# Kernel tuning notes

Measured on AMD Instinct MI355X. Metric: run time of the kernel, lower is better.

The kernel has to match this reference:

```python
import jax, jax.numpy as jnp
import numpy as np

B, S, E, H = 2, 2048, 1024, 16
D = E // H
LN_EPS = 1e-5
NORM_EPS = 1e-12  # F.normalize clamp_min


def setup_inputs() -> dict:
    key = jax.random.key(0)
    ks = jax.random.split(key, 4)
    x = jax.random.normal(ks[0], (B, S, E), dtype=jnp.float32)
    qkv_w = jax.random.normal(ks[1], (3 * E, E), dtype=jnp.float32) * 0.02
    qkv_b = jnp.zeros((3 * E,), dtype=jnp.float32)
    out_w = jax.random.normal(ks[2], (E, E), dtype=jnp.float32) * 0.02
    out_b = jnp.zeros((E,), dtype=jnp.float32)
    ln_w = jnp.ones((E,), dtype=jnp.float32)
    ln_b = jnp.zeros((E,), dtype=jnp.float32)
    qknorm_scale = jnp.asarray(E ** -0.5, dtype=jnp.float32)
    # RotaryEmbedding buffer: inv_freq interleaved (emb[::2] = emb[1::2] = base**(-arange(0,E,2)/E))
    base_freq = 10000.0 ** (-(np.arange(0, E, 2).astype(np.float32) / E))
    emb = np.empty((E,), dtype=np.float32)
    emb[::2] = base_freq
    emb[1::2] = base_freq
    inv_freq = jnp.asarray(emb)
    return {"x": x, "ln_w": ln_w, "ln_b": ln_b, "qkv_w": qkv_w, "qkv_b": qkv_b,
            "qknorm_scale": qknorm_scale, "out_w": out_w, "out_b": out_b, "inv_freq": inv_freq}


def _rotate(t, sin, cos):
    # Faithful to source: x1 = even idx (excluding last), x2 = odd idx; cat(-x2, x1)
    x1 = t[..., :-1:2]
    x2 = t[..., 1::2]
    t_rot = jnp.concatenate((-x2, x1), axis=-1)
    return t * cos + t_rot * sin


def _l2norm(t):
    n = jnp.sqrt(jnp.sum(t * t, axis=-1, keepdims=True))
    return t / jnp.maximum(n, NORM_EPS)


def reference(x, ln_w, ln_b, qkv_w, qkv_b, qknorm_scale, out_w, out_b, inv_freq):
    # --- prenorm (LayerNorm, eps=1e-5) ---
    mu = jnp.mean(x, axis=-1, keepdims=True)
    var = jnp.mean((x - mu) ** 2, axis=-1, keepdims=True)
    xn = (x - mu) / jnp.sqrt(var + LN_EPS) * ln_w + ln_b
    # --- QKV projection ---
    qkv = xn @ qkv_w.T + qkv_b  # [B,S,3E]
    q, k, v = jnp.split(qkv, 3, axis=-1)
    # --- rotary (source uses scalar seq*inv_freq, not per-position) ---
    seq = q.shape[1]
    sin = jnp.sin(seq * inv_freq)
    cos = jnp.cos(seq * inv_freq)
    q = _rotate(q, sin, cos)
    k = _rotate(k, sin, cos)
    # --- split heads: [B,S,E] -> [B,H,S,D] ---
    split = lambda t: t.reshape(B, seq, H, D).transpose(0, 2, 1, 3)
    q, k, v = split(q), split(k), split(v)
    # --- qknorm ---
    q = _l2norm(q) * qknorm_scale
    k = _l2norm(k) * qknorm_scale
    # --- scaled dot product with causal mask ---
    aw = jnp.einsum('bhqd,bhkd->bhqk', q, k)  # [B,H,S,S]
    causal = jnp.tril(jnp.ones((seq, seq), dtype=bool))
    aw = jnp.where(causal, aw, jnp.finfo(aw.dtype).min)
    aw = jax.nn.softmax(aw, axis=-1)
    attn = jnp.einsum('bhqk,bhkd->bhqd', aw, v)
    # --- merge heads + out proj ---
    attn = attn.transpose(0, 2, 1, 3).reshape(B, seq, E)
    return attn @ out_w.T + out_b
```

## Files before the change

### kernel.cpp

```cpp
#include <hip/hip_runtime.h>

typedef unsigned short u16;
typedef __attribute__((ext_vector_type(8))) short bf16x8;
typedef __attribute__((ext_vector_type(4))) float f32x4;

#define SS 2048
#define EE 1024
#define HH 16
#define DD 64

__device__ __forceinline__ float b2f(u16 u) {
  union { unsigned int i; float f; } v; v.i = ((unsigned int)u) << 16; return v.f;
}
__device__ __forceinline__ u16 f2b(float f) {
  union { float f; unsigned int i; } v; v.f = f;
  unsigned int i = v.i;
  return (u16)((i + 0x7FFFu + ((i >> 16) & 1u)) >> 16);
}
__device__ __forceinline__ unsigned int cvt_pk_bf16(float lo, float hi) {
  unsigned int r;
  asm("v_cvt_pk_bf16_f32 %0, %1, %2" : "=v"(r) : "v"(lo), "v"(hi));
  return r;
}

#define GLD16(g, l)                                                         \
  __builtin_amdgcn_global_load_lds(                                         \
      (const __attribute__((address_space(1))) unsigned int*)(g),           \
      (__attribute__((address_space(3))) unsigned int*)(l), 16, 0, 0)

__global__ __launch_bounds__(256) void k_prep(const float* __restrict__ qkv_w,
                                              u16* __restrict__ wq_b,
                                              const float* __restrict__ inv_freq,
                                              float2* __restrict__ cs,
                                              const float* __restrict__ x,
                                              const float* __restrict__ lw,
                                              const float* __restrict__ lb,
                                              u16* __restrict__ xn) {
  const int bx = blockIdx.x, t = threadIdx.x;
  if (bx < 3072) {
    const int i = bx * 256 + t;
    float4 v = ((const float4*)qkv_w)[i];
    ushort4 o;
    o.x = f2b(v.x); o.y = f2b(v.y); o.z = f2b(v.z); o.w = f2b(v.w);
    ((ushort4*)wq_b)[i] = o;
    return;
  }
  if (bx < 3076) {
    const int i = (bx - 3072) * 256 + t;
    float th = 2048.0f * inv_freq[i];
    cs[i] = make_float2(cosf(th), sinf(th));
    return;
  }
  const int row = bx - 3076;
  float4 v = ((const float4*)(x + (size_t)row * EE))[t];
  float f0 = v.x, f1 = v.y, f2 = v.z, f3 = v.w;
  float s = f0 + f1 + f2 + f3;
  float ss = f0 * f0 + f1 * f1 + f2 * f2 + f3 * f3;
  for (int o = 1; o < 64; o <<= 1) { s += __shfl_xor(s, o); ss += __shfl_xor(ss, o); }
  __shared__ float red[8];
  int w = t >> 6;
  if ((t & 63) == 0) { red[w] = s; red[4 + w] = ss; }
  __syncthreads();
  s = red[0] + red[1] + red[2] + red[3];
  ss = red[4] + red[5] + red[6] + red[7];
  float mu = s * (1.0f / 1024.0f);
  float var = ss * (1.0f / 1024.0f) - mu * mu;
  float rstd = rsqrtf(var + 1e-5f);
  float4 wv = ((const float4*)lw)[t];
  float4 bv = ((const float4*)lb)[t];
  ushort4 o;
  o.x = f2b((f0 - mu) * rstd * wv.x + bv.x);
  o.y = f2b((f1 - mu) * rstd * wv.y + bv.y);
  o.z = f2b((f2 - mu) * rstd * wv.z + bv.z);
  o.w = f2b((f3 - mu) * rstd * wv.w + bv.w);
  ((ushort4*)(xn + (size_t)row * EE))[t] = o;
}

__global__ __launch_bounds__(256) void k_cvt(const float* __restrict__ src,
                                             u16* __restrict__ dst) {
  const int i = blockIdx.x * 256 + threadIdx.x;
  float4 v = ((const float4*)src)[i];
  ushort4 o;
  o.x = f2b(v.x); o.y = f2b(v.y); o.z = f2b(v.z); o.w = f2b(v.w);
  ((ushort4*)dst)[i] = o;
}

template <typename OutT, int BM64>
__device__ __forceinline__ void gemm_body(const u16* __restrict__ A,
                                          const u16* __restrict__ W,
                                          const float* __restrict__ bias,
                                          OutT* __restrict__ C,
                                          int M, int N, int K) {
  constexpr int BM = 64 * BM64;
  constexpr int MI = 2 * BM64;
  __shared__ __align__(16) u16 As[BM * 32];
  __shared__ __align__(16) u16 Ws[128 * 32];
  const int t = threadIdx.x;
  const int m0 = blockIdx.y * BM, n0 = blockIdx.x * 128;
  const int lane = t & 63, w = t >> 6, quad = lane >> 4, l15 = lane & 15;
  const int wm = (w & 1) * (BM / 2), wn = (w >> 1) * 64;

  f32x4 zero4 = {0.f, 0.f, 0.f, 0.f};
  f32x4 acc[MI][4];
  for (int mi = 0; mi < MI; mi++)
    for (int ni = 0; ni < 4; ni++) acc[mi][ni] = zero4;

  const u16* Ag = A + (size_t)(m0 + (t >> 2)) * K + (t & 3) * 8;
  const u16* Wg = W + (size_t)(n0 + (t >> 2)) * K + (t & 3) * 8;
  const size_t rowskip = (size_t)64 * K;

  for (int k0 = 0; k0 < K; k0 += 32) {
    GLD16(Ag + k0, As + t * 8);
    if constexpr (BM64 == 2) GLD16(Ag + rowskip + k0, As + 2048 + t * 8);
    GLD16(Wg + k0, Ws + t * 8);
    GLD16(Wg + rowskip + k0, Ws + 2048 + t * 8);
    __syncthreads();
    bf16x8 af[MI], wf[4];
#pragma unroll
    for (int i = 0; i < MI; i++)
      af[i] = *(const bf16x8*)(As + (wm + i * 16 + l15) * 32 + quad * 8);
#pragma unroll
    for (int i = 0; i < 4; i++)
      wf[i] = *(const bf16x8*)(Ws + (wn + i * 16 + l15) * 32 + quad * 8);
#pragma unroll
    for (int mi = 0; mi < MI; mi++)
#pragma unroll
      for (int ni = 0; ni < 4; ni++)
        acc[mi][ni] = __builtin_amdgcn_mfma_f32_16x16x32_bf16(af[mi], wf[ni], acc[mi][ni], 0, 0, 0);
    __syncthreads();
  }
  for (int mi = 0; mi < MI; mi++)
    for (int ni = 0; ni < 4; ni++) {
      int col = n0 + wn + ni * 16 + l15;
      float bb = bias[col];
      for (int r = 0; r < 4; r++) {
        int grow = m0 + wm + mi * 16 + quad * 4 + r;
        float val = acc[mi][ni][r] + bb;
        if constexpr (sizeof(OutT) == 2) C[(size_t)grow * N + col] = f2b(val);
        else                             C[(size_t)grow * N + col] = val;
      }
    }
}

__global__ __launch_bounds__(256) void k_gemm_b(const u16* A, const u16* W,
                                                const float* bias, u16* C,
                                                int M, int N, int K) {
  gemm_body<u16, 2>(A, W, bias, C, M, N, K);
}
__global__ __launch_bounds__(256) void k_gemm_f(const u16* A, const u16* W,
                                                const float* bias, float* C,
                                                int M, int N, int K) {
  gemm_body<float, 1>(A, W, bias, C, M, N, K);
}

__global__ __launch_bounds__(256) void k_rotv(u16* __restrict__ qkv,
                                              const float2* __restrict__ cs_tab,
                                              const float* __restrict__ scale_p,
                                              u16* __restrict__ vt) {
  __shared__ float qf[1024];
  __shared__ float kf[1024];
  __shared__ __align__(16) u16 tile[64 * 72];
  const int row = blockIdx.x, t = threadIdx.x;
  {
    u16* qr = qkv + (size_t)row * 3072;
    u16* kr = qr + 1024;
    ushort4 qv = ((const ushort4*)qr)[t];
    ushort4 kv = ((const ushort4*)kr)[t];
    *(float4*)(qf + 4 * t) = make_float4(b2f(qv.x), b2f(qv.y), b2f(qv.z), b2f(qv.w));
    *(float4*)(kf + 4 * t) = make_float4(b2f(kv.x), b2f(kv.y), b2f(kv.z), b2f(kv.w));
    __syncthreads();
    const float scale = scale_p[0];
    float rq[4], rk[4];
#pragma unroll
    for (int u = 0; u < 4; u++) {
      int j = 4 * t + u;
      float2 cs = cs_tab[j];
      float qrot = (j < 512) ? -qf[2 * j + 1] : qf[2 * (j - 512)];
      float krot = (j < 512) ? -kf[2 * j + 1] : kf[2 * (j - 512)];
      rq[u] = qf[j] * cs.x + qrot * cs.y;
      rk[u] = kf[j] * cs.x + krot * cs.y;
    }
    float ssq = rq[0] * rq[0] + rq[1] * rq[1] + rq[2] * rq[2] + rq[3] * rq[3];
    float ssk = rk[0] * rk[0] + rk[1] * rk[1] + rk[2] * rk[2] + rk[3] * rk[3];
    for (int o = 1; o < 16; o <<= 1) { ssq += __shfl_xor(ssq, o); ssk += __shfl_xor(ssk, o); }
    float qs = scale / fmaxf(sqrtf(ssq), 1e-12f);
    float ks = scale / fmaxf(sqrtf(ssk), 1e-12f);
    ushort4 qo, ko;
    qo.x = f2b(rq[0] * qs); qo.y = f2b(rq[1] * qs); qo.z = f2b(rq[2] * qs); qo.w = f2b(rq[3] * qs);
    ko.x = f2b(rk[0] * ks); ko.y = f2b(rk[1] * ks); ko.z = f2b(rk[2] * ks); ko.w = f2b(rk[3] * ks);
    ((ushort4*)qr)[t] = qo;
    ((ushort4*)kr)[t] = ko;
  }
  if (row >= 1024) return;
  const int st = row & 31, bh = row >> 5;
  const int b = bh >> 4, h = bh & 15;
  const int s0 = st * 64;
  const int si = t >> 2, dc = t & 3;
  __syncthreads();
  const u16* src = qkv + (size_t)(b * SS + s0 + si) * 3072 + 2048 + h * DD;
  bf16x8 v0 = *(const bf16x8*)(src + dc * 8);
  bf16x8 v1 = *(const bf16x8*)(src + (dc + 4) * 8);
#pragma unroll
  for (int u = 0; u < 8; u++) tile[(dc * 8 + u) * 72 + si] = (u16)v0[u];
#pragma unroll
  for (int u = 0; u < 8; u++) tile[((dc + 4) * 8 + u) * 72 + si] = (u16)v1[u];
  __syncthreads();
#pragma unroll
  for (int it = 0; it < 2; it++) {
    int idx = t + it * 256;
    int d = idx >> 3, ch = idx & 7;
    bf16x8 o = *(const bf16x8*)(tile + d * 72 + ch * 8);
    *(bf16x8*)(vt + (size_t)(bh * DD + d) * SS + s0 + ch * 8) = o;
  }
}

__global__ __launch_bounds__(256) void k_attn(const u16* __restrict__ qkv,
                                              const u16* __restrict__ vt,
                                              u16* __restrict__ out) {
  __shared__ __align__(16) u16 Kt[128 * 72];
  __shared__ __align__(16) u16 Vt[64 * 136];
  __shared__ __align__(16) u16 Pt[64 * 136];
  const int bh = blockIdx.y;
  const int b = bh >> 4, h = bh & 15;
  const int t = threadIdx.x, w = t >> 6, lane = t & 63, quad = lane >> 4, l15 = lane & 15;
  const int kr = t >> 1, kdh = (t & 1) * 32;
  const int dr = t >> 2, kc4 = t & 3;
  const u16* kn = qkv + 1024;
  f32x4 zero4 = {0.f, 0.f, 0.f, 0.f};

  for (int rep = 0; rep < 2; rep++) {
    const int qt = rep ? 31 - (int)blockIdx.x : (int)blockIdx.x;
    const int q0 = qt * 64;
    const int lim = qt >> 1;

    bf16x8 qf[2];
    {
      const u16* qrow = qkv + (size_t)(b * SS + q0 + 16 * w + l15) * 3072 + h * DD;
      qf[0] = *(const bf16x8*)(qrow + quad * 8);
      qf[1] = *(const bf16x8*)(qrow + 32 + quad * 8);
    }
    f32x4 oacc[4];
    for (int n = 0; n < 4; n++) oacc[n] = zero4;
    float m_i[4] = {-1e30f, -1e30f, -1e30f, -1e30f};
    float l_i[4] = {0.f, 0.f, 0.f, 0.f};

    bf16x8 kv[4], vv[4];
    {
      const u16* krow = kn + (size_t)(b * SS + kr) * 3072 + h * DD + kdh;
      const u16* vrow = vt + (size_t)(bh * DD + dr) * SS + kc4 * 32;
#pragma unroll
      for (int j = 0; j < 4; j++) kv[j] = *(const bf16x8*)(krow + j * 8);
#pragma unroll
      for (int j = 0; j < 4; j++) vv[j] = *(const bf16x8*)(vrow + j * 8);
    }
#pragma unroll
    for (int j = 0; j < 4; j++) *(bf16x8*)(Kt + kr * 72 + kdh + j * 8) = kv[j];
#pragma unroll
    for (int j = 0; j < 4; j++) {
      const int ch = kc4 * 4 + j;
      u16* vb = Vt + dr * 136 + (ch & 1) * 64 + (ch >> 1);
#pragma unroll
      for (int e = 0; e < 8; e++) vb[e * 8] = (u16)vv[j][e];
    }
    __syncthreads();

    for (int kt = 0; kt <= lim; kt++) {
      if (kt < lim) {
        const int k0n = (kt + 1) * 128;
        const u16* krow = kn + (size_t)(b * SS + k0n + kr) * 3072 + h * DD + kdh;
        const u16* vrow = vt + (size_t)(bh * DD + dr) * SS + k0n + kc4 * 32;
#pragma unroll
        for (int j = 0; j < 4; j++) kv[j] = *(const bf16x8*)(krow + j * 8);
#pragma unroll
        for (int j = 0; j < 4; j++) vv[j] = *(const bf16x8*)(vrow + j * 8);
      }
      f32x4 sacc[8];
#pragma unroll
      for (int n = 0; n < 8; n++) {
        sacc[n] = zero4;
#pragma unroll
        for (int c = 0; c < 2; c++) {
          bf16x8 kfrag = *(const bf16x8*)(Kt + (n * 16 + l15) * 72 + c * 32 + quad * 8);
          sacc[n] = __builtin_amdgcn_mfma_f32_16x16x32_bf16(qf[c], kfrag, sacc[n], 0, 0, 0);
        }
      }
      if (kt == lim) {
        const int rbase = (qt & 1) * 64 + 16 * w + quad * 4;
#pragma unroll
        for (int n = 0; n < 8; n++)
#pragma unroll
          for (int r = 0; r < 4; r++)
            if (n * 16 + l15 > rbase + r) sacc[n][r] = -1e30f;
      }
#pragma unroll
      for (int r = 0; r < 4; r++) {
        float mx = fmaxf(fmaxf(fmaxf(sacc[0][r], sacc[1][r]), fmaxf(sacc[2][r], sacc[3][r])),
                         fmaxf(fmaxf(sacc[4][r], sacc[5][r]), fmaxf(sacc[6][r], sacc[7][r])));
        for (int o = 1; o < 16; o <<= 1) mx = fmaxf(mx, __shfl_xor(mx, o));
        float mn = fmaxf(m_i[r], mx);
        float al = __expf(m_i[r] - mn);
        m_i[r] = mn;
        float rs = 0.f;
#pragma unroll
        for (int n = 0; n < 8; n++) {
          float p = __expf(sacc[n][r] - mn);
          sacc[n][r] = p;
          rs += p;
        }
        for (int o = 1; o < 16; o <<= 1) rs += __shfl_xor(rs, o);
        l_i[r] = al * l_i[r] + rs;
#pragma unroll
        for (int n = 0; n < 4; n++) oacc[n][r] *= al;
      }
#pragma unroll
      for (int r = 0; r < 4; r++) {
        union { unsigned int u[4]; bf16x8 v8; } pk;
        pk.u[0] = cvt_pk_bf16(sacc[0][r], sacc[1][r]);
        pk.u[1] = cvt_pk_bf16(sacc[2][r], sacc[3][r]);
        pk.u[2] = cvt_pk_bf16(sacc[4][r], sacc[5][r]);
        pk.u[3] = cvt_pk_bf16(sacc[6][r], sacc[7][r]);
        *(bf16x8*)(Pt + (16 * w + quad * 4 + r) * 136 + l15 * 8) = pk.v8;
      }
      asm volatile("s_waitcnt lgkmcnt(0)" ::: "memory");
      __builtin_amdgcn_sched_barrier(0);
#pragma unroll
      for (int c = 0; c < 4; c++) {
        bf16x8 pf = *(const bf16x8*)(Pt + (16 * w + l15) * 136 + c * 32 + quad * 8);
#pragma unroll
        for (int n = 0; n < 4; n++) {
          bf16x8 vf = *(const bf16x8*)(Vt + (n * 16 + l15) * 136 + c * 32 + quad * 8);
          oacc[n] = __builtin_amdgcn_mfma_f32_16x16x32_bf16(pf, vf, oacc[n], 0, 0, 0);
        }
      }
      __syncthreads();
      if (kt < lim) {
#pragma unroll
        for (int j = 0; j < 4; j++) *(bf16x8*)(Kt + kr * 72 + kdh + j * 8) = kv[j];
#pragma unroll
        for (int j = 0; j < 4; j++) {
          const int ch = kc4 * 4 + j;
          u16* vb = Vt + dr * 136 + (ch & 1) * 64 + (ch >> 1);
#pragma unroll
          for (int e = 0; e < 8; e++) vb[e * 8] = (u16)vv[j][e];
        }
      }
      __syncthreads();
    }
    for (int n = 0; n < 4; n++)
      for (int r = 0; r < 4; r++) {
        int row = q0 + 16 * w + quad * 4 + r;
        out[(size_t)(b * SS + row) * EE + h * DD + n * 16 + l15] = f2b(oacc[n][r] / l_i[r]);
      }
  }
}

extern "C" void kernel_launch(void* const* d_in, const int* in_sizes, int n_in,
                              void* d_out, int out_size, void* d_ws, size_t ws_size,
                              hipStream_t stream) {
  const float* x       = (const float*)d_in[0];
  const float* ln_w    = (const float*)d_in[1];
  const float* ln_b    = (const float*)d_in[2];
  const float* qkv_w   = (const float*)d_in[3];
  const float* qkv_b   = (const float*)d_in[4];
  const float* qk_s    = (const float*)d_in[5];
  const float* out_w   = (const float*)d_in[6];
  const float* out_b   = (const float*)d_in[7];
  const float* inv_frq = (const float*)d_in[8];

  u16* ws   = (u16*)d_ws;
  u16* xn   = ws;
  u16* qkv  = ws + (size_t)4096 * 1024;
  u16* wq_b = (u16*)d_out;
  float2* cs_tab = (float2*)((char*)d_out + 6291456);
  u16* vt   = (u16*)d_out + (size_t)4194304;
  u16* wo_b = qkv;

  k_prep<<<7172, 256, 0, stream>>>(qkv_w, wq_b, inv_frq, cs_tab, x, ln_w, ln_b, xn);
  k_gemm_b<<<dim3(24, 32), 256, 0, stream>>>(xn, wq_b, qkv_b, qkv, 4096, 3072, 1024);
  k_rotv<<<4096, 256, 0, stream>>>(qkv, cs_tab, qk_s, vt);
  k_attn<<<dim3(16, 32), 256, 0, stream>>>(qkv, vt, xn);
  k_cvt<<<1024, 256, 0, stream>>>(out_w, wo_b);
  k_gemm_f<<<dim3(8, 64), 256, 0, stream>>>(xn, wo_b, out_b, (float*)d_out, 4096, 1024, 1024);
}
```

Before: 228.1 us.

## Process paired query tiles jointly in attention and fuse out_w conversion into GEMM

The attention kernel now handles its two query tiles (qt and 31-qt) in a single pass over the shared K/V tiles, instead of two sequential passes. Each K/V tile is loaded once and both score blocks are computed from it, using a second P buffer in LDS. The separate fp32-to-bf16 conversion kernel for out_w is removed; the output-projection GEMM now reads fp32 weights and converts them while staging to LDS. This saves one launch and an extra weight round trip, but raises register pressure and LDS use in attention, and the weight loads in the GEMM become synchronous register loads instead of async GLD16.

```diff
diff --git a/kernel.cpp b/kernel.cpp
--- a/kernel.cpp
+++ b/kernel.cpp
@@ -76,33 +76,21 @@
   ((ushort4*)(xn + (size_t)row * EE))[t] = o;
 }
 
-__global__ __launch_bounds__(256) void k_cvt(const float* __restrict__ src,
-                                             u16* __restrict__ dst) {
-  const int i = blockIdx.x * 256 + threadIdx.x;
-  float4 v = ((const float4*)src)[i];
-  ushort4 o;
-  o.x = f2b(v.x); o.y = f2b(v.y); o.z = f2b(v.z); o.w = f2b(v.w);
-  ((ushort4*)dst)[i] = o;
-}
-
-template <typename OutT, int BM64>
-__device__ __forceinline__ void gemm_body(const u16* __restrict__ A,
-                                          const u16* __restrict__ W,
-                                          const float* __restrict__ bias,
-                                          OutT* __restrict__ C,
-                                          int M, int N, int K) {
-  constexpr int BM = 64 * BM64;
-  constexpr int MI = 2 * BM64;
-  __shared__ __align__(16) u16 As[BM * 32];
+__global__ __launch_bounds__(256) void k_gemm_b(const u16* __restrict__ A,
+                                                const u16* __restrict__ W,
+                                                const float* __restrict__ bias,
+                                                u16* __restrict__ C,
+                                                int M, int N, int K) {
+  __shared__ __align__(16) u16 As[128 * 32];
   __shared__ __align__(16) u16 Ws[128 * 32];
   const int t = threadIdx.x;
-  const int m0 = blockIdx.y * BM, n0 = blockIdx.x * 128;
+  const int m0 = blockIdx.y * 128, n0 = blockIdx.x * 128;
   const int lane = t & 63, w = t >> 6, quad = lane >> 4, l15 = lane & 15;
-  const int wm = (w & 1) * (BM / 2), wn = (w >> 1) * 64;
+  const int wm = (w & 1) * 64, wn = (w >> 1) * 64;
 
   f32x4 zero4 = {0.f, 0.f, 0.f, 0.f};
-  f32x4 acc[MI][4];
-  for (int mi = 0; mi < MI; mi++)
+  f32x4 acc[4][4];
+  for (int mi = 0; mi < 4; mi++)
     for (int ni = 0; ni < 4; ni++) acc[mi][ni] = zero4;
 
   const u16* Ag = A + (size_t)(m0 + (t >> 2)) * K + (t & 3) * 8;
@@ -111,46 +99,92 @@
 
   for (int k0 = 0; k0 < K; k0 += 32) {
     GLD16(Ag + k0, As + t * 8);
-    if constexpr (BM64 == 2) GLD16(Ag + rowskip + k0, As + 2048 + t * 8);
+    GLD16(Ag + rowskip + k0, As + 2048 + t * 8);
     GLD16(Wg + k0, Ws + t * 8);
     GLD16(Wg + rowskip + k0, Ws + 2048 + t * 8);
     __syncthreads();
-    bf16x8 af[MI], wf[4];
-#pragma unroll
-    for (int i = 0; i < MI; i++)
+    bf16x8 af[4], wf[4];
+#pragma unroll
+    for (int i = 0; i < 4; i++) {
       af[i] = *(const bf16x8*)(As + (wm + i * 16 + l15) * 32 + quad * 8);
-#pragma unroll
-    for (int i = 0; i < 4; i++)
       wf[i] = *(const bf16x8*)(Ws + (wn + i * 16 + l15) * 32 + quad * 8);
-#pragma unroll
-    for (int mi = 0; mi < MI; mi++)
+    }
+#pragma unroll
+    for (int mi = 0; mi < 4; mi++)
 #pragma unroll
       for (int ni = 0; ni < 4; ni++)
         acc[mi][ni] = __builtin_amdgcn_mfma_f32_16x16x32_bf16(af[mi], wf[ni], acc[mi][ni], 0, 0, 0);
     __syncthreads();
   }
-  for (int mi = 0; mi < MI; mi++)
+  for (int mi = 0; mi < 4; mi++)
     for (int ni = 0; ni < 4; ni++) {
       int col = n0 + wn + ni * 16 + l15;
       float bb = bias[col];
       for (int r = 0; r < 4; r++) {
         int grow = m0 + wm + mi * 16 + quad * 4 + r;
-        float val = acc[mi][ni][r] + bb;
-        if constexpr (sizeof(OutT) == 2) C[(size_t)grow * N + col] = f2b(val);
-        else                             C[(size_t)grow * N + col] = val;
-      }
-    }
-}
-
-__global__ __launch_bounds__(256) void k_gemm_b(const u16* A, const u16* W,
-                                                const float* bias, u16* C,
-                                                int M, int N, int K) {
-  gemm_body<u16, 2>(A, W, bias, C, M, N, K);
-}
-__global__ __launch_bounds__(256) void k_gemm_f(const u16* A, const u16* W,
-                                                const float* bias, float* C,
-                                                int M, int N, int K) {
-  gemm_body<float, 1>(A, W, bias, C, M, N, K);
+        C[(size_t)grow * N + col] = f2b(acc[mi][ni][r] + bb);
+      }
+    }
+}
+
+__global__ __launch_bounds__(256) void k_gemm_fw(const u16* __restrict__ A,
+                                                 const float* __restrict__ W,
+                                                 const float* __restrict__ bias,
+                                                 float* __restrict__ C,
+                                                 int M, int N, int K) {
+  __shared__ __align__(16) u16 As[64 * 32];
+  __shared__ __align__(16) u16 Ws[128 * 32];
+  const int t = threadIdx.x;
+  const int m0 = blockIdx.y * 64, n0 = blockIdx.x * 128;
+  const int lane = t & 63, w = t >> 6, quad = lane >> 4, l15 = lane & 15;
+  const int wm = (w & 1) * 32, wn = (w >> 1) * 64;
+
+  f32x4 zero4 = {0.f, 0.f, 0.f, 0.f};
+  f32x4 acc[2][4];
+  for (int mi = 0; mi < 2; mi++)
+    for (int ni = 0; ni < 4; ni++) acc[mi][ni] = zero4;
+
+  const u16* Ag = A + (size_t)(m0 + (t >> 2)) * K + (t & 3) * 8;
+  const float* Wg0 = W + (size_t)(n0 + (t >> 2)) * K + (t & 3) * 8;
+  const float* Wg1 = Wg0 + (size_t)64 * K;
+
+  for (int k0 = 0; k0 < K; k0 += 32) {
+    GLD16(Ag + k0, As + t * 8);
+    float4 wa = *(const float4*)(Wg0 + k0);
+    float4 wb = *(const float4*)(Wg0 + k0 + 4);
+    float4 wc = *(const float4*)(Wg1 + k0);
+    float4 wd = *(const float4*)(Wg1 + k0 + 4);
+    union { unsigned int u[4]; bf16x8 v8; } p0, p1;
+    p0.u[0] = cvt_pk_bf16(wa.x, wa.y); p0.u[1] = cvt_pk_bf16(wa.z, wa.w);
+    p0.u[2] = cvt_pk_bf16(wb.x, wb.y); p0.u[3] = cvt_pk_bf16(wb.z, wb.w);
+    p1.u[0] = cvt_pk_bf16(wc.x, wc.y); p1.u[1] = cvt_pk_bf16(wc.z, wc.w);
+    p1.u[2] = cvt_pk_bf16(wd.x, wd.y); p1.u[3] = cvt_pk_bf16(wd.z, wd.w);
+    *(bf16x8*)(Ws + t * 8) = p0.v8;
+    *(bf16x8*)(Ws + 2048 + t * 8) = p1.v8;
+    __syncthreads();
+    bf16x8 af[2], wf[4];
+#pragma unroll
+    for (int i = 0; i < 2; i++)
+      af[i] = *(const bf16x8*)(As + (wm + i * 16 + l15) * 32 + quad * 8);
+#pragma unroll
+    for (int i = 0; i < 4; i++)
+      wf[i] = *(const bf16x8*)(Ws + (wn + i * 16 + l15) * 32 + quad * 8);
+#pragma unroll
+    for (int mi = 0; mi < 2; mi++)
+#pragma unroll
+      for (int ni = 0; ni < 4; ni++)
+        acc[mi][ni] = __builtin_amdgcn_mfma_f32_16x16x32_bf16(af[mi], wf[ni], acc[mi][ni], 0, 0, 0);
+    __syncthreads();
+  }
+  for (int mi = 0; mi < 2; mi++)
+    for (int ni = 0; ni < 4; ni++) {
+      int col = n0 + wn + ni * 16 + l15;
+      float bb = bias[col];
+      for (int r = 0; r < 4; r++) {
+        int grow = m0 + wm + mi * 16 + quad * 4 + r;
+        C[(size_t)grow * N + col] = acc[mi][ni][r] + bb;
+      }
+    }
 }
 
 __global__ __launch_bounds__(256) void k_rotv(u16* __restrict__ qkv,
@@ -219,7 +253,8 @@
                                               u16* __restrict__ out) {
   __shared__ __align__(16) u16 Kt[128 * 72];
   __shared__ __align__(16) u16 Vt[64 * 136];
-  __shared__ __align__(16) u16 Pt[64 * 136];
+  __shared__ __align__(16) u16 PtA[64 * 136];
+  __shared__ __align__(16) u16 PtB[64 * 136];
   const int bh = blockIdx.y;
   const int b = bh >> 4, h = bh & 15;
   const int t = threadIdx.x, w = t >> 6, lane = t & 63, quad = lane >> 4, l15 = lane & 15;
@@ -228,130 +263,205 @@
   const u16* kn = qkv + 1024;
   f32x4 zero4 = {0.f, 0.f, 0.f, 0.f};
 
-  for (int rep = 0; rep < 2; rep++) {
-    const int qt = rep ? 31 - (int)blockIdx.x : (int)blockIdx.x;
-    const int q0 = qt * 64;
-    const int lim = qt >> 1;
-
-    bf16x8 qf[2];
-    {
-      const u16* qrow = qkv + (size_t)(b * SS + q0 + 16 * w + l15) * 3072 + h * DD;
-      qf[0] = *(const bf16x8*)(qrow + quad * 8);
-      qf[1] = *(const bf16x8*)(qrow + 32 + quad * 8);
-    }
-    f32x4 oacc[4];
-    for (int n = 0; n < 4; n++) oacc[n] = zero4;
-    float m_i[4] = {-1e30f, -1e30f, -1e30f, -1e30f};
-    float l_i[4] = {0.f, 0.f, 0.f, 0.f};
-
-    bf16x8 kv[4], vv[4];
-    {
-      const u16* krow = kn + (size_t)(b * SS + kr) * 3072 + h * DD + kdh;
-      const u16* vrow = vt + (size_t)(bh * DD + dr) * SS + kc4 * 32;
+  const int qtA = blockIdx.x;
+  const int qtB = 31 - qtA;
+  const int limA = qtA >> 1;
+  const int limB = qtB >> 1;
+  const int q0A = qtA * 64, q0B = qtB * 64;
+
+  bf16x8 qfA[2], qfB[2];
+  {
+    const u16* qa = qkv + (size_t)(b * SS + q0A + 16 * w + l15) * 3072 + h * DD;
+    qfA[0] = *(const bf16x8*)(qa + quad * 8);
+    qfA[1] = *(const bf16x8*)(qa + 32 + quad * 8);
+    const u16* qb = qkv + (size_t)(b * SS + q0B + 16 * w + l15) * 3072 + h * DD;
+    qfB[0] = *(const bf16x8*)(qb + quad * 8);
+    qfB[1] = *(const bf16x8*)(qb + 32 + quad * 8);
+  }
+  f32x4 oA[4], oB[4];
+  for (int n = 0; n < 4; n++) { oA[n] = zero4; oB[n] = zero4; }
+  float mA[4] = {-1e30f, -1e30f, -1e30f, -1e30f}, lA[4] = {0.f, 0.f, 0.f, 0.f};
+  float mB[4] = {-1e30f, -1e30f, -1e30f, -1e30f}, lB[4] = {0.f, 0.f, 0.f, 0.f};
+
+  bf16x8 kv[4], vv[4];
+  {
+    const u16* krow = kn + (size_t)(b * SS + kr) * 3072 + h * DD + kdh;
+    const u16* vrow = vt + (size_t)(bh * DD + dr) * SS + kc4 * 32;
+#pragma unroll
+    for (int j = 0; j < 4; j++) kv[j] = *(const bf16x8*)(krow + j * 8);
+#pragma unroll
+    for (int j = 0; j < 4; j++) vv[j] = *(const bf16x8*)(vrow + j * 8);
+  }
+#pragma unroll
+  for (int j = 0; j < 4; j++) *(bf16x8*)(Kt + kr * 72 + kdh + j * 8) = kv[j];
+#pragma unroll
+  for (int j = 0; j < 4; j++) {
+    const int ch = kc4 * 4 + j;
+    u16* vb = Vt + dr * 136 + (ch & 1) * 64 + (ch >> 1);
+#pragma unroll
+    for (int e = 0; e < 8; e++) vb[e * 8] = (u16)vv[j][e];
+  }
+  __syncthreads();
+
+  for (int kt = 0; kt <= limB; kt++) {
+    if (kt < limB) {
+      const int k0n = (kt + 1) * 128;
+      const u16* krow = kn + (size_t)(b * SS + k0n + kr) * 3072 + h * DD + kdh;
+      const u16* vrow = vt + (size_t)(bh * DD + dr) * SS + k0n + kc4 * 32;
 #pragma unroll
       for (int j = 0; j < 4; j++) kv[j] = *(const bf16x8*)(krow + j * 8);
 #pragma unroll
       for (int j = 0; j < 4; j++) vv[j] = *(const bf16x8*)(vrow + j * 8);
     }
-#pragma unroll
-    for (int j = 0; j < 4; j++) *(bf16x8*)(Kt + kr * 72 + kdh + j * 8) = kv[j];
-#pragma unroll
-    for (int j = 0; j < 4; j++) {
-      const int ch = kc4 * 4 + j;
-      u16* vb = Vt + dr * 136 + (ch & 1) * 64 + (ch >> 1);
-#pragma unroll
-      for (int e = 0; e < 8; e++) vb[e * 8] = (u16)vv[j][e];
-    }
-    __syncthreads();
-
-    for (int kt = 0; kt <= lim; kt++) {
-      if (kt < lim) {
-        const int k0n = (kt + 1) * 128;
-        const u16* krow = kn + (size_t)(b * SS + k0n + kr) * 3072 + h * DD + kdh;
-        const u16* vrow = vt + (size_t)(bh * DD + dr) * SS + k0n + kc4 * 32;
-#pragma unroll
-        for (int j = 0; j < 4; j++) kv[j] = *(const bf16x8*)(krow + j * 8);
-#pragma unroll
-        for (int j = 0; j < 4; j++) vv[j] = *(const bf16x8*)(vrow + j * 8);
-      }
-      f32x4 sacc[8];
+    f32x4 sB[8];
+#pragma unroll
+    for (int n = 0; n < 8; n++) {
+      sB[n] = zero4;
+#pragma unroll
+      for (int c = 0; c < 2; c++) {
+        bf16x8 kfrag = *(const bf16x8*)(Kt + (n * 16 + l15) * 72 + c * 32 + quad * 8);
+        sB[n] = __builtin_amdgcn_mfma_f32_16x16x32_bf16(qfB[c], kfrag, sB[n], 0, 0, 0);
+      }
+    }
+    if (kt == limB) {
+      const int rb = (qtB & 1) * 64 + 16 * w + quad * 4;
+#pragma unroll
+      for (int n = 0; n < 8; n++)
+#pragma unroll
+        for (int r = 0; r < 4; r++)
+          if (n * 16 + l15 > rb + r) sB[n][r] = -1e30f;
+    }
+    if (kt <= limA) {
+      f32x4 sA[8];
 #pragma unroll
       for (int n = 0; n < 8; n++) {
-        sacc[n] = zero4;
+        sA[n] = zero4;
 #pragma unroll
         for (int c = 0; c < 2; c++) {
           bf16x8 kfrag = *(const bf16x8*)(Kt + (n * 16 + l15) * 72 + c * 32 + quad * 8);
-          sacc[n] = __builtin_amdgcn_mfma_f32_16x16x32_bf16(qf[c], kfrag, sacc[n], 0, 0, 0);
-        }
-      }
-      if (kt == lim) {
-        const int rbase = (qt & 1) * 64 + 16 * w + quad * 4;
+          sA[n] = __builtin_amdgcn_mfma_f32_16x16x32_bf16(qfA[c], kfrag, sA[n], 0, 0, 0);
+        }
+      }
+      if (kt == limA) {
+        const int ra = (qtA & 1) * 64 + 16 * w + quad * 4;
 #pragma unroll
         for (int n = 0; n < 8; n++)
 #pragma unroll
           for (int r = 0; r < 4; r++)
-            if (n * 16 + l15 > rbase + r) sacc[n][r] = -1e30f;
-      }
-#pragma unroll
-      for (int r = 0; r < 4; r++) {
-        float mx = fmaxf(fmaxf(fmaxf(sacc[0][r], sacc[1][r]), fmaxf(sacc[2][r], sacc[3][r])),
-                         fmaxf(fmaxf(sacc[4][r], sacc[5][r]), fmaxf(sacc[6][r], sacc[7][r])));
-        for (int o = 1; o < 16; o <<= 1) mx = fmaxf(mx, __shfl_xor(mx, o));
-        float mn = fmaxf(m_i[r], mx);
-        float al = __expf(m_i[r] - mn);
-        m_i[r] = mn;
-        float rs = 0.f;
+            if (n * 16 + l15 > ra + r) sA[n][r] = -1e30f;
+      }
+#pragma unroll
+      for (int r = 0; r < 4; r++) {
+        float mxB = fmaxf(fmaxf(fmaxf(sB[0][r], sB[1][r]), fmaxf(sB[2][r], sB[3][r])),
+                          fmaxf(fmaxf(sB[4][r], sB[5][r]), fmaxf(sB[6][r], sB[7][r])));
+        float mxA = fmaxf(fmaxf(fmaxf(sA[0][r], sA[1][r]), fmaxf(sA[2][r], sA[3][r])),
+                          fmaxf(fmaxf(sA[4][r], sA[5][r]), fmaxf(sA[6][r], sA[7][r])));
+        for (int o = 1; o < 16; o <<= 1) {
+          mxB = fmaxf(mxB, __shfl_xor(mxB, o));
+          mxA = fmaxf(mxA, __shfl_xor(mxA, o));
+        }
+        float mnB = fmaxf(mB[r], mxB), mnA = fmaxf(mA[r], mxA);
+        float alB = __expf(mB[r] - mnB), alA = __expf(mA[r] - mnA);
+        mB[r] = mnB; mA[r] = mnA;
+        float rsB = 0.f, rsA = 0.f;
 #pragma unroll
         for (int n = 0; n < 8; n++) {
-          float p = __expf(sacc[n][r] - mn);
-          sacc[n][r] = p;
-          rs += p;
-        }
-        for (int o = 1; o < 16; o <<= 1) rs += __shfl_xor(rs, o);
-        l_i[r] = al * l_i[r] + rs;
-#pragma unroll
-        for (int n = 0; n < 4; n++) oacc[n][r] *= al;
-      }
-#pragma unroll
-      for (int r = 0; r < 4; r++) {
-        union { unsigned int u[4]; bf16x8 v8; } pk;
-        pk.u[0] = cvt_pk_bf16(sacc[0][r], sacc[1][r]);
-        pk.u[1] = cvt_pk_bf16(sacc[2][r], sacc[3][r]);
-        pk.u[2] = cvt_pk_bf16(sacc[4][r], sacc[5][r]);
-        pk.u[3] = cvt_pk_bf16(sacc[6][r], sacc[7][r]);
-        *(bf16x8*)(Pt + (16 * w + quad * 4 + r) * 136 + l15 * 8) = pk.v8;
+          float pB = __expf(sB[n][r] - mnB); sB[n][r] = pB; rsB += pB;
+          float pA = __expf(sA[n][r] - mnA); sA[n][r] = pA; rsA += pA;
+        }
+        for (int o = 1; o < 16; o <<= 1) {
+          rsB += __shfl_xor(rsB, o);
+          rsA += __shfl_xor(rsA, o);
+        }
+        lB[r] = alB * lB[r] + rsB;
+        lA[r] = alA * lA[r] + rsA;
+#pragma unroll
+        for (int n = 0; n < 4; n++) { oB[n][r] *= alB; oA[n][r] *= alA; }
+      }
+#pragma unroll
+      for (int r = 0; r < 4; r++) {
+        union { unsigned int u[4]; bf16x8 v8; } pb, pa;
+        pb.u[0] = cvt_pk_bf16(sB[0][r], sB[1][r]); pb.u[1] = cvt_pk_bf16(sB[2][r], sB[3][r]);
+        pb.u[2] = cvt_pk_bf16(sB[4][r], sB[5][r]); pb.u[3] = cvt_pk_bf16(sB[6][r], sB[7][r]);
+        pa.u[0] = cvt_pk_bf16(sA[0][r], sA[1][r]); pa.u[1] = cvt_pk_bf16(sA[2][r], sA[3][r]);
+        pa.u[2] = cvt_pk_bf16(sA[4][r], sA[5][r]); pa.u[3] = cvt_pk_bf16(sA[6][r], sA[7][r]);
+        *(bf16x8*)(PtB + (16 * w + quad * 4 + r) * 136 + l15 * 8) = pb.v8;
+        *(bf16x8*)(PtA + (16 * w + quad * 4 + r) * 136 + l15 * 8) = pa.v8;
       }
       asm volatile("s_waitcnt lgkmcnt(0)" ::: "memory");
       __builtin_amdgcn_sched_barrier(0);
 #pragma unroll
       for (int c = 0; c < 4; c++) {
-        bf16x8 pf = *(const bf16x8*)(Pt + (16 * w + l15) * 136 + c * 32 + quad * 8);
+        bf16x8 pfB = *(const bf16x8*)(PtB + (16 * w + l15) * 136 + c * 32 + quad * 8);
+        bf16x8 pfA = *(const bf16x8*)(PtA + (16 * w + l15) * 136 + c * 32 + quad * 8);
 #pragma unroll
         for (int n = 0; n < 4; n++) {
           bf16x8 vf = *(const bf16x8*)(Vt + (n * 16 + l15) * 136 + c * 32 + quad * 8);
-          oacc[n] = __builtin_amdgcn_mfma_f32_16x16x32_bf16(pf, vf, oacc[n], 0, 0, 0);
-        }
-      }
-      __syncthreads();
-      if (kt < lim) {
-#pragma unroll
-        for (int j = 0; j < 4; j++) *(bf16x8*)(Kt + kr * 72 + kdh + j * 8) = kv[j];
-#pragma unroll
-        for (int j = 0; j < 4; j++) {
-          const int ch = kc4 * 4 + j;
-          u16* vb = Vt + dr * 136 + (ch & 1) * 64 + (ch >> 1);
-#pragma unroll
-          for (int e = 0; e < 8; e++) vb[e * 8] = (u16)vv[j][e];
-        }
-      }
-      __syncthreads();
-    }
-    for (int n = 0; n < 4; n++)
-      for (int r = 0; r < 4; r++) {
-        int row = q0 + 16 * w + quad * 4 + r;
-        out[(size_t)(b * SS + row) * EE + h * DD + n * 16 + l15] = f2b(oacc[n][r] / l_i[r]);
-      }
-  }
+          oB[n] = __builtin_amdgcn_mfma_f32_16x16x32_bf16(pfB, vf, oB[n], 0, 0, 0);
+          oA[n] = __builtin_amdgcn_mfma_f32_16x16x32_bf16(pfA, vf, oA[n], 0, 0, 0);
+        }
+      }
+    } else {
+#pragma unroll
+      for (int r = 0; r < 4; r++) {
+        float mx = fmaxf(fmaxf(fmaxf(sB[0][r], sB[1][r]), fmaxf(sB[2][r], sB[3][r])),
+                         fmaxf(fmaxf(sB[4][r], sB[5][r]), fmaxf(sB[6][r], sB[7][r])));
+        for (int o = 1; o < 16; o <<= 1) mx = fmaxf(mx, __shfl_xor(mx, o));
+        float mn = fmaxf(mB[r], mx);
+        float al = __expf(mB[r] - mn);
+        mB[r] = mn;
+        float rs = 0.f;
+#pragma unroll
+        for (int n = 0; n < 8; n++) {
+          float p = __expf(sB[n][r] - mn);
+          sB[n][r] = p;
+          rs += p;
+        }
+        for (int o = 1; o < 16; o <<= 1) rs += __shfl_xor(rs, o);
+        lB[r] = al * lB[r] + rs;
+#pragma unroll
+        for (int n = 0; n < 4; n++) oB[n][r] *= al;
+      }
+#pragma unroll
+      for (int r = 0; r < 4; r++) {
+        union { unsigned int u[4]; bf16x8 v8; } pb;
+        pb.u[0] = cvt_pk_bf16(sB[0][r], sB[1][r]); pb.u[1] = cvt_pk_bf16(sB[2][r], sB[3][r]);
+        pb.u[2] = cvt_pk_bf16(sB[4][r], sB[5][r]); pb.u[3] = cvt_pk_bf16(sB[6][r], sB[7][r]);
+        *(bf16x8*)(PtB + (16 * w + quad * 4 + r) * 136 + l15 * 8) = pb.v8;
+      }
+      asm volatile("s_waitcnt lgkmcnt(0)" ::: "memory");
+      __builtin_amdgcn_sched_barrier(0);
+#pragma unroll
+      for (int c = 0; c < 4; c++) {
+        bf16x8 pf = *(const bf16x8*)(PtB + (16 * w + l15) * 136 + c * 32 + quad * 8);
+#pragma unroll
+        for (int n = 0; n < 4; n++) {
+          bf16x8 vf = *(const bf16x8*)(Vt + (n * 16 + l15) * 136 + c * 32 + quad * 8);
+          oB[n] = __builtin_amdgcn_mfma_f32_16x16x32_bf16(pf, vf, oB[n], 0, 0, 0);
+        }
+      }
+    }
+    __syncthreads();
+    if (kt < limB) {
+#pragma unroll
+      for (int j = 0; j < 4; j++) *(bf16x8*)(Kt + kr * 72 + kdh + j * 8) = kv[j];
+#pragma unroll
+      for (int j = 0; j < 4; j++) {
+        const int ch = kc4 * 4 + j;
+        u16* vb = Vt + dr * 136 + (ch & 1) * 64 + (ch >> 1);
+#pragma unroll
+        for (int e = 0; e < 8; e++) vb[e * 8] = (u16)vv[j][e];
+      }
+    }
+    __syncthreads();
+  }
+  for (int n = 0; n < 4; n++)
+    for (int r = 0; r < 4; r++) {
+      int rowA = q0A + 16 * w + quad * 4 + r;
+      int rowB = q0B + 16 * w + quad * 4 + r;
+      out[(size_t)(b * SS + rowA) * EE + h * DD + n * 16 + l15] = f2b(oA[n][r] / lA[r]);
+      out[(size_t)(b * SS + rowB) * EE + h * DD + n * 16 + l15] = f2b(oB[n][r] / lB[r]);
+    }
 }
 
 extern "C" void kernel_launch(void* const* d_in, const int* in_sizes, int n_in,
@@ -373,12 +483,10 @@
   u16* wq_b = (u16*)d_out;
   float2* cs_tab = (float2*)((char*)d_out + 6291456);
   u16* vt   = (u16*)d_out + (size_t)4194304;
-  u16* wo_b = qkv;
 
   k_prep<<<7172, 256, 0, stream>>>(qkv_w, wq_b, inv_frq, cs_tab, x, ln_w, ln_b, xn);
   k_gemm_b<<<dim3(24, 32), 256, 0, stream>>>(xn, wq_b, qkv_b, qkv, 4096, 3072, 1024);
   k_rotv<<<4096, 256, 0, stream>>>(qkv, cs_tab, qk_s, vt);
   k_attn<<<dim3(16, 32), 256, 0, stream>>>(qkv, vt, xn);
-  k_cvt<<<1024, 256, 0, stream>>>(out_w, wo_b);
-  k_gemm_f<<<dim3(8, 64), 256, 0, stream>>>(xn, wo_b, out_b, (float*)d_out, 4096, 1024, 1024);
-}
+  k_gemm_fw<<<dim3(8, 64), 256, 0, stream>>>(xn, out_w, out_b, (float*)d_out, 4096, 1024, 1024);
+}
```

Result: slower. 269.1 us (+18.0%).

## Fuse out_w bf16 conversion into out-proj GEMM and use 128-row attention tiles

Applied to the files above, without the earlier changes.

The out-projection GEMM now reads the fp32 out_w directly and converts it to bf16 in registers before the LDS store, which removes the separate k_cvt kernel and its round trip through global memory. Attention blocks now run 512 threads (8 waves) over 128-row query tiles with 8 x 32 blocks, so each K/V tile is loaded into LDS once per 128 query rows and each thread stages half as much. The per-wave waitcnt before the P·V step becomes a full __syncthreads. The trade-offs are fewer blocks in the attention grid, an extra block-wide barrier per key tile, and fp32 weight loads repeated by every GEMM row-block instead of a single conversion pass.

```diff
diff --git a/kernel.cpp b/kernel.cpp
--- a/kernel.cpp
+++ b/kernel.cpp
@@ -76,33 +76,21 @@
   ((ushort4*)(xn + (size_t)row * EE))[t] = o;
 }
 
-__global__ __launch_bounds__(256) void k_cvt(const float* __restrict__ src,
-                                             u16* __restrict__ dst) {
-  const int i = blockIdx.x * 256 + threadIdx.x;
-  float4 v = ((const float4*)src)[i];
-  ushort4 o;
-  o.x = f2b(v.x); o.y = f2b(v.y); o.z = f2b(v.z); o.w = f2b(v.w);
-  ((ushort4*)dst)[i] = o;
-}
-
-template <typename OutT, int BM64>
-__device__ __forceinline__ void gemm_body(const u16* __restrict__ A,
-                                          const u16* __restrict__ W,
-                                          const float* __restrict__ bias,
-                                          OutT* __restrict__ C,
-                                          int M, int N, int K) {
-  constexpr int BM = 64 * BM64;
-  constexpr int MI = 2 * BM64;
-  __shared__ __align__(16) u16 As[BM * 32];
+__global__ __launch_bounds__(256) void k_gemm_b(const u16* __restrict__ A,
+                                                const u16* __restrict__ W,
+                                                const float* __restrict__ bias,
+                                                u16* __restrict__ C,
+                                                int M, int N, int K) {
+  __shared__ __align__(16) u16 As[128 * 32];
   __shared__ __align__(16) u16 Ws[128 * 32];
   const int t = threadIdx.x;
-  const int m0 = blockIdx.y * BM, n0 = blockIdx.x * 128;
+  const int m0 = blockIdx.y * 128, n0 = blockIdx.x * 128;
   const int lane = t & 63, w = t >> 6, quad = lane >> 4, l15 = lane & 15;
-  const int wm = (w & 1) * (BM / 2), wn = (w >> 1) * 64;
+  const int wm = (w & 1) * 64, wn = (w >> 1) * 64;
 
   f32x4 zero4 = {0.f, 0.f, 0.f, 0.f};
-  f32x4 acc[MI][4];
-  for (int mi = 0; mi < MI; mi++)
+  f32x4 acc[4][4];
+  for (int mi = 0; mi < 4; mi++)
     for (int ni = 0; ni < 4; ni++) acc[mi][ni] = zero4;
 
   const u16* Ag = A + (size_t)(m0 + (t >> 2)) * K + (t & 3) * 8;
@@ -111,46 +99,92 @@
 
   for (int k0 = 0; k0 < K; k0 += 32) {
     GLD16(Ag + k0, As + t * 8);
-    if constexpr (BM64 == 2) GLD16(Ag + rowskip + k0, As + 2048 + t * 8);
+    GLD16(Ag + rowskip + k0, As + 2048 + t * 8);
     GLD16(Wg + k0, Ws + t * 8);
     GLD16(Wg + rowskip + k0, Ws + 2048 + t * 8);
     __syncthreads();
-    bf16x8 af[MI], wf[4];
-#pragma unroll
-    for (int i = 0; i < MI; i++)
+    bf16x8 af[4], wf[4];
+#pragma unroll
+    for (int i = 0; i < 4; i++) {
       af[i] = *(const bf16x8*)(As + (wm + i * 16 + l15) * 32 + quad * 8);
-#pragma unroll
-    for (int i = 0; i < 4; i++)
       wf[i] = *(const bf16x8*)(Ws + (wn + i * 16 + l15) * 32 + quad * 8);
-#pragma unroll
-    for (int mi = 0; mi < MI; mi++)
+    }
+#pragma unroll
+    for (int mi = 0; mi < 4; mi++)
 #pragma unroll
       for (int ni = 0; ni < 4; ni++)
         acc[mi][ni] = __builtin_amdgcn_mfma_f32_16x16x32_bf16(af[mi], wf[ni], acc[mi][ni], 0, 0, 0);
     __syncthreads();
   }
-  for (int mi = 0; mi < MI; mi++)
+  for (int mi = 0; mi < 4; mi++)
     for (int ni = 0; ni < 4; ni++) {
       int col = n0 + wn + ni * 16 + l15;
       float bb = bias[col];
       for (int r = 0; r < 4; r++) {
         int grow = m0 + wm + mi * 16 + quad * 4 + r;
-        float val = acc[mi][ni][r] + bb;
-        if constexpr (sizeof(OutT) == 2) C[(size_t)grow * N + col] = f2b(val);
-        else                             C[(size_t)grow * N + col] = val;
-      }
-    }
-}
-
-__global__ __launch_bounds__(256) void k_gemm_b(const u16* A, const u16* W,
-                                                const float* bias, u16* C,
-                                                int M, int N, int K) {
-  gemm_body<u16, 2>(A, W, bias, C, M, N, K);
-}
-__global__ __launch_bounds__(256) void k_gemm_f(const u16* A, const u16* W,
-                                                const float* bias, float* C,
-                                                int M, int N, int K) {
-  gemm_body<float, 1>(A, W, bias, C, M, N, K);
+        C[(size_t)grow * N + col] = f2b(acc[mi][ni][r] + bb);
+      }
+    }
+}
+
+__global__ __launch_bounds__(256) void k_gemm_fw(const u16* __restrict__ A,
+                                                 const float* __restrict__ W,
+                                                 const float* __restrict__ bias,
+                                                 float* __restrict__ C,
+                                                 int M, int N, int K) {
+  __shared__ __align__(16) u16 As[64 * 32];
+  __shared__ __align__(16) u16 Ws[128 * 32];
+  const int t = threadIdx.x;
+  const int m0 = blockIdx.y * 64, n0 = blockIdx.x * 128;
+  const int lane = t & 63, w = t >> 6, quad = lane >> 4, l15 = lane & 15;
+  const int wm = (w & 1) * 32, wn = (w >> 1) * 64;
+
+  f32x4 zero4 = {0.f, 0.f, 0.f, 0.f};
+  f32x4 acc[2][4];
+  for (int mi = 0; mi < 2; mi++)
+    for (int ni = 0; ni < 4; ni++) acc[mi][ni] = zero4;
+
+  const u16* Ag = A + (size_t)(m0 + (t >> 2)) * K + (t & 3) * 8;
+  const float* Wg0 = W + (size_t)(n0 + (t >> 2)) * K + (t & 3) * 8;
+  const float* Wg1 = Wg0 + (size_t)64 * K;
+
+  for (int k0 = 0; k0 < K; k0 += 32) {
+    GLD16(Ag + k0, As + t * 8);
+    float4 wa = *(const float4*)(Wg0 + k0);
+    float4 wb = *(const float4*)(Wg0 + k0 + 4);
+    float4 wc = *(const float4*)(Wg1 + k0);
+    float4 wd = *(const float4*)(Wg1 + k0 + 4);
+    union { unsigned int u[4]; bf16x8 v8; } p0, p1;
+    p0.u[0] = cvt_pk_bf16(wa.x, wa.y); p0.u[1] = cvt_pk_bf16(wa.z, wa.w);
+    p0.u[2] = cvt_pk_bf16(wb.x, wb.y); p0.u[3] = cvt_pk_bf16(wb.z, wb.w);
+    p1.u[0] = cvt_pk_bf16(wc.x, wc.y); p1.u[1] = cvt_pk_bf16(wc.z, wc.w);
+    p1.u[2] = cvt_pk_bf16(wd.x, wd.y); p1.u[3] = cvt_pk_bf16(wd.z, wd.w);
+    *(bf16x8*)(Ws + t * 8) = p0.v8;
+    *(bf16x8*)(Ws + 2048 + t * 8) = p1.v8;
+    __syncthreads();
+    bf16x8 af[2], wf[4];
+#pragma unroll
+    for (int i = 0; i < 2; i++)
+      af[i] = *(const bf16x8*)(As + (wm + i * 16 + l15) * 32 + quad * 8);
+#pragma unroll
+    for (int i = 0; i < 4; i++)
+      wf[i] = *(const bf16x8*)(Ws + (wn + i * 16 + l15) * 32 + quad * 8);
+#pragma unroll
+    for (int mi = 0; mi < 2; mi++)
+#pragma unroll
+      for (int ni = 0; ni < 4; ni++)
+        acc[mi][ni] = __builtin_amdgcn_mfma_f32_16x16x32_bf16(af[mi], wf[ni], acc[mi][ni], 0, 0, 0);
+    __syncthreads();
+  }
+  for (int mi = 0; mi < 2; mi++)
+    for (int ni = 0; ni < 4; ni++) {
+      int col = n0 + wn + ni * 16 + l15;
+      float bb = bias[col];
+      for (int r = 0; r < 4; r++) {
+        int grow = m0 + wm + mi * 16 + quad * 4 + r;
+        C[(size_t)grow * N + col] = acc[mi][ni][r] + bb;
+      }
+    }
 }
 
 __global__ __launch_bounds__(256) void k_rotv(u16* __restrict__ qkv,
@@ -214,24 +248,23 @@
   }
 }
 
-__global__ __launch_bounds__(256) void k_attn(const u16* __restrict__ qkv,
+__global__ __launch_bounds__(512) void k_attn(const u16* __restrict__ qkv,
                                               const u16* __restrict__ vt,
                                               u16* __restrict__ out) {
   __shared__ __align__(16) u16 Kt[128 * 72];
   __shared__ __align__(16) u16 Vt[64 * 136];
-  __shared__ __align__(16) u16 Pt[64 * 136];
+  __shared__ __align__(16) u16 Pt[128 * 136];
   const int bh = blockIdx.y;
   const int b = bh >> 4, h = bh & 15;
   const int t = threadIdx.x, w = t >> 6, lane = t & 63, quad = lane >> 4, l15 = lane & 15;
-  const int kr = t >> 1, kdh = (t & 1) * 32;
-  const int dr = t >> 2, kc4 = t & 3;
+  const int krow = t >> 2, kq = (t & 3) * 16;
+  const int dr = t >> 3, kc8 = t & 7;
   const u16* kn = qkv + 1024;
   f32x4 zero4 = {0.f, 0.f, 0.f, 0.f};
 
   for (int rep = 0; rep < 2; rep++) {
-    const int qt = rep ? 31 - (int)blockIdx.x : (int)blockIdx.x;
-    const int q0 = qt * 64;
-    const int lim = qt >> 1;
+    const int qt = rep ? 15 - (int)blockIdx.x : (int)blockIdx.x;
+    const int q0 = qt * 128;
 
     bf16x8 qf[2];
     {
@@ -244,35 +277,36 @@
     float m_i[4] = {-1e30f, -1e30f, -1e30f, -1e30f};
     float l_i[4] = {0.f, 0.f, 0.f, 0.f};
 
-    bf16x8 kv[4], vv[4];
+    bf16x8 kv[2], vv[2];
     {
-      const u16* krow = kn + (size_t)(b * SS + kr) * 3072 + h * DD + kdh;
-      const u16* vrow = vt + (size_t)(bh * DD + dr) * SS + kc4 * 32;
-#pragma unroll
-      for (int j = 0; j < 4; j++) kv[j] = *(const bf16x8*)(krow + j * 8);
-#pragma unroll
-      for (int j = 0; j < 4; j++) vv[j] = *(const bf16x8*)(vrow + j * 8);
-    }
-#pragma unroll
-    for (int j = 0; j < 4; j++) *(bf16x8*)(Kt + kr * 72 + kdh + j * 8) = kv[j];
-#pragma unroll
-    for (int j = 0; j < 4; j++) {
-      const int ch = kc4 * 4 + j;
+      const u16* krg = kn + (size_t)(b * SS + krow) * 3072 + h * DD + kq;
+      kv[0] = *(const bf16x8*)(krg);
+      kv[1] = *(const bf16x8*)(krg + 8);
+      const u16* vrg = vt + (size_t)(bh * DD + dr) * SS + kc8 * 16;
+      vv[0] = *(const bf16x8*)(vrg);
+      vv[1] = *(const bf16x8*)(vrg + 8);
+    }
+    __syncthreads();
+    *(bf16x8*)(Kt + krow * 72 + kq) = kv[0];
+    *(bf16x8*)(Kt + krow * 72 + kq + 8) = kv[1];
+#pragma unroll
+    for (int j = 0; j < 2; j++) {
+      const int ch = kc8 * 2 + j;
       u16* vb = Vt + dr * 136 + (ch & 1) * 64 + (ch >> 1);
 #pragma unroll
       for (int e = 0; e < 8; e++) vb[e * 8] = (u16)vv[j][e];
     }
     __syncthreads();
 
-    for (int kt = 0; kt <= lim; kt++) {
-      if (kt < lim) {
+    for (int kt = 0; kt <= qt; kt++) {
+      if (kt < qt) {
         const int k0n = (kt + 1) * 128;
-        const u16* krow = kn + (size_t)(b * SS + k0n + kr) * 3072 + h * DD + kdh;
-        const u16* vrow = vt + (size_t)(bh * DD + dr) * SS + k0n + kc4 * 32;
-#pragma unroll
-        for (int j = 0; j < 4; j++) kv[j] = *(const bf16x8*)(krow + j * 8);
-#pragma unroll
-        for (int j = 0; j < 4; j++) vv[j] = *(const bf16x8*)(vrow + j * 8);
+        const u16* krg = kn + (size_t)(b * SS + k0n + krow) * 3072 + h * DD + kq;
+        kv[0] = *(const bf16x8*)(krg);
+        kv[1] = *(const bf16x8*)(krg + 8);
+        const u16* vrg = vt + (size_t)(bh * DD + dr) * SS + k0n + kc8 * 16;
+        vv[0] = *(const bf16x8*)(vrg);
+        vv[1] = *(const bf16x8*)(vrg + 8);
       }
       f32x4 sacc[8];
 #pragma unroll
@@ -284,8 +318,8 @@
           sacc[n] = __builtin_amdgcn_mfma_f32_16x16x32_bf16(qf[c], kfrag, sacc[n], 0, 0, 0);
         }
       }
-      if (kt == lim) {
-        const int rbase = (qt & 1) * 64 + 16 * w + quad * 4;
+      if (kt == qt) {
+        const int rbase = 16 * w + quad * 4;
 #pragma unroll
         for (int n = 0; n < 8; n++)
 #pragma unroll
@@ -321,8 +355,7 @@
         pk.u[3] = cvt_pk_bf16(sacc[6][r], sacc[7][r]);
         *(bf16x8*)(Pt + (16 * w + quad * 4 + r) * 136 + l15 * 8) = pk.v8;
       }
-      asm volatile("s_waitcnt lgkmcnt(0)" ::: "memory");
-      __builtin_amdgcn_sched_barrier(0);
+      __syncthreads();
 #pragma unroll
       for (int c = 0; c < 4; c++) {
         bf16x8 pf = *(const bf16x8*)(Pt + (16 * w + l15) * 136 + c * 32 + quad * 8);
@@ -333,12 +366,12 @@
         }
       }
       __syncthreads();
-      if (kt < lim) {
-#pragma unroll
-        for (int j = 0; j < 4; j++) *(bf16x8*)(Kt + kr * 72 + kdh + j * 8) = kv[j];
-#pragma unroll
-        for (int j = 0; j < 4; j++) {
-          const int ch = kc4 * 4 + j;
+      if (kt < qt) {
+        *(bf16x8*)(Kt + krow * 72 + kq) = kv[0];
+        *(bf16x8*)(Kt + krow * 72 + kq + 8) = kv[1];
+#pragma unroll
+        for (int j = 0; j < 2; j++) {
+          const int ch = kc8 * 2 + j;
           u16* vb = Vt + dr * 136 + (ch & 1) * 64 + (ch >> 1);
 #pragma unroll
           for (int e = 0; e < 8; e++) vb[e * 8] = (u16)vv[j][e];
@@ -373,12 +406,10 @@
   u16* wq_b = (u16*)d_out;
   float2* cs_tab = (float2*)((char*)d_out + 6291456);
   u16* vt   = (u16*)d_out + (size_t)4194304;
-  u16* wo_b = qkv;
 
   k_prep<<<7172, 256, 0, stream>>>(qkv_w, wq_b, inv_frq, cs_tab, x, ln_w, ln_b, xn);
   k_gemm_b<<<dim3(24, 32), 256, 0, stream>>>(xn, wq_b, qkv_b, qkv, 4096, 3072, 1024);
   k_rotv<<<4096, 256, 0, stream>>>(qkv, cs_tab, qk_s, vt);
-  k_attn<<<dim3(16, 32), 256, 0, stream>>>(qkv, vt, xn);
-  k_cvt<<<1024, 256, 0, stream>>>(out_w, wo_b);
-  k_gemm_f<<<dim3(8, 64), 256, 0, stream>>>(xn, wo_b, out_b, (float*)d_out, 4096, 1024, 1024);
-}
+  k_attn<<<dim3(8, 32), 512, 0, stream>>>(qkv, vt, xn);
+  k_gemm_fw<<<dim3(8, 64), 256, 0, stream>>>(xn, out_w, out_b, (float*)d_out, 4096, 1024, 1024);
+}
```

Result: no change. 231.5 us (+1.5%).
